# Performance work log

Measured on AMD Instinct MI355X. Metric: run time of the kernel, lower is better.

## Reference

```python
import jax, jax.numpy as jnp
import numpy as np

BS, SEQ, C = 8, 1024, 1024

def setup_inputs() -> dict:
    key = jax.random.key(0)
    ks = jax.random.split(key, 5)
    inp = {
        "input": jax.random.normal(ks[0], (BS, SEQ, C), dtype=jnp.float32),
        "Wq": jax.random.normal(ks[1], (C, C), dtype=jnp.float32) * 0.001,
        "Wk": jax.random.normal(ks[2], (C, C), dtype=jnp.float32) * 0.001,
        "Wv": jax.random.normal(ks[3], (C, C), dtype=jnp.float32) * 0.001,
        "bq": jnp.zeros((C,), dtype=jnp.float32),
        "bk": jnp.zeros((C,), dtype=jnp.float32),
        "bv": jnp.zeros((C,), dtype=jnp.float32),
        "bias_position": jnp.ones((SEQ, SEQ), dtype=jnp.float32),
    }
    return inp

def reference(input, Wq, Wk, Wv, bq, bk, bv, bias_position):
    # Linear layers (torch nn.Linear: x @ W.T + b)
    q = input @ Wq.T + bq                      # (bs, seq, c)
    k = input @ Wk.T + bk                      # (bs, seq, c)
    v = input @ Wv.T + bv                      # (bs, seq, c)
    # AFT: out[b,t,c] = sum_s exp(k[b,s,c] + bias[t,s]) * v[b,s,c]
    #                 / sum_s exp(k[b,s,c] + bias[t,s])
    # Factor exp(k + bias) = exp(bias) * exp(k) -> two GEMM-like einsums,
    # avoiding the (seq, bs, seq, c) intermediate of the original.
    ek = jnp.exp(k)                            # (bs, seq, c)
    eb = jnp.exp(bias_position)                # (t, s)
    numerator = jnp.einsum('ts,bsc->btc', eb, ek * v)   # (bs, t, c)
    denominator = jnp.einsum('ts,bsc->btc', eb, ek)     # (bs, t, c)
    out = jax.nn.sigmoid(q) * (numerator / denominator)
    return out
```

## Files before the change

kernel.cpp:

```cpp
#include <hip/hip_runtime.h>

#define BSZ 8
#define SEQL 1024
#define CHN 1024
#define M1 (BSZ*SEQL)

typedef __attribute__((ext_vector_type(8))) short bf16x8;
typedef __attribute__((ext_vector_type(4))) float f32x4;
typedef __attribute__((ext_vector_type(4))) unsigned short us4;
typedef __attribute__((ext_vector_type(8))) unsigned short us8;

static __device__ __forceinline__ unsigned short f2bf(float f){
  unsigned int u = __float_as_uint(f);
  u += 0x7fffu + ((u >> 16) & 1u);
  return (unsigned short)(u >> 16);
}
static __device__ __forceinline__ float bf2f(unsigned short h){
  return __uint_as_float(((unsigned int)h) << 16);
}
static __device__ __forceinline__ void gload16(const void* g, void* l){
  __builtin_amdgcn_global_load_lds((const __attribute__((address_space(1))) void*)g,
                                   (__attribute__((address_space(3))) void*)l,
                                   16, 0, 0);
}

__global__ void prep_kernel(const float* __restrict__ x, const float* __restrict__ wq,
                            const float* __restrict__ wk, const float* __restrict__ wv,
                            const float* __restrict__ bias,
                            unsigned short* __restrict__ xb, unsigned short* __restrict__ wqb,
                            unsigned short* __restrict__ wkb, unsigned short* __restrict__ wvb,
                            unsigned short* __restrict__ ebb)
{
  const int NX = M1 * CHN;
  const int NW = CHN * CHN;
  const int total4 = (NX + 3 * NW + SEQL * SEQL) >> 2;
  for (int i = blockIdx.x * blockDim.x + threadIdx.x; i < total4;
       i += gridDim.x * blockDim.x) {
    int e = i << 2;
    const float* src; unsigned short* dst; int off; bool ex = false;
    if (e < NX)               { src = x;    dst = xb;  off = e; }
    else if (e < NX + NW)     { src = wq;   dst = wqb; off = e - NX; }
    else if (e < NX + 2 * NW) { src = wk;   dst = wkb; off = e - (NX + NW); }
    else if (e < NX + 3 * NW) { src = wv;   dst = wvb; off = e - (NX + 2 * NW); }
    else                      { src = bias; dst = ebb; off = e - (NX + 3 * NW); ex = true; }
    float4 v = *reinterpret_cast<const float4*>(src + off);
    if (ex) { v.x = expf(v.x); v.y = expf(v.y); v.z = expf(v.z); v.w = expf(v.w); }
    us4 o; o.x = f2bf(v.x); o.y = f2bf(v.y); o.z = f2bf(v.z); o.w = f2bf(v.w);
    *reinterpret_cast<us4*>(dst + off) = o;
  }
}

__global__ __launch_bounds__(256) void gemm_qkv(
    const unsigned short* __restrict__ Xb,
    const unsigned short* __restrict__ Wq, const unsigned short* __restrict__ Wk,
    const unsigned short* __restrict__ Wv,
    const float* __restrict__ bq, const float* __restrict__ bk,
    const float* __restrict__ bv,
    unsigned short* __restrict__ Qb,
    unsigned short* __restrict__ EKT, unsigned short* __restrict__ EKVT)
{
  __shared__ unsigned short lds[20480];
  const int tid = threadIdx.x;
  const int lane = tid & 63;
  const int wm = tid >> 7;
  const int wn = (tid >> 6) & 1;
  const int nwg = gridDim.x;
  const int lid = blockIdx.x;
  const int sid = (lid & 7) * (nwg >> 3) + (lid >> 3);
  const int m0 = (sid >> 4) * 128;
  const int n0 = (sid & 15) * 64;

  const unsigned short* srcA[4]; unsigned short* dstA[4];
#pragma unroll
  for (int p = 0; p < 4; p++) {
    int l = p * 4096 + tid * 16;
    int row = l >> 7;
    int lc = ((l >> 4) & 7) ^ (row & 7);
    srcA[p] = Xb + (m0 + row) * CHN + lc * 8;
    dstA[p] = lds + (l >> 1);
  }
  const unsigned short* Ws0 = Wq; const unsigned short* Ws1 = Wk; const unsigned short* Ws2 = Wv;
  const unsigned short* srcB[3][2]; unsigned short* dstB[3][2];
#pragma unroll
  for (int w = 0; w < 3; w++) {
    const unsigned short* W = (w == 0) ? Ws0 : (w == 1) ? Ws1 : Ws2;
#pragma unroll
    for (int p = 0; p < 2; p++) {
      int l = p * 4096 + tid * 16;
      int row = l >> 7;
      int lc = ((l >> 4) & 7) ^ (row & 7);
      srcB[w][p] = W + (n0 + row) * CHN + lc * 8;
      dstB[w][p] = lds + 8192 + w * 4096 + (l >> 1);
    }
  }

  int aOff[4][2], bOff[2][2];
#pragma unroll
  for (int mi = 0; mi < 4; mi++) {
    int r = wm * 64 + mi * 16 + (lane & 15);
#pragma unroll
    for (int ks = 0; ks < 2; ks++)
      aOff[mi][ks] = r * 64 + ((((ks << 2) + (lane >> 4)) ^ (r & 7)) << 3);
  }
#pragma unroll
  for (int ni = 0; ni < 2; ni++) {
    int r = wn * 32 + ni * 16 + (lane & 15);
#pragma unroll
    for (int ks = 0; ks < 2; ks++)
      bOff[ni][ks] = r * 64 + ((((ks << 2) + (lane >> 4)) ^ (r & 7)) << 3);
  }

  f32x4 accq[4][2] = {}, acck[4][2] = {}, accv[4][2] = {};

  for (int kk = 0; kk < CHN; kk += 64) {
#pragma unroll
    for (int p = 0; p < 4; p++) gload16(srcA[p] + kk, dstA[p]);
#pragma unroll
    for (int w = 0; w < 3; w++)
#pragma unroll
      for (int p = 0; p < 2; p++) gload16(srcB[w][p] + kk, dstB[w][p]);
    __syncthreads();
#pragma unroll
    for (int ks = 0; ks < 2; ks++) {
      bf16x8 af[4];
#pragma unroll
      for (int mi = 0; mi < 4; mi++)
        af[mi] = *reinterpret_cast<const bf16x8*>(lds + aOff[mi][ks]);
#pragma unroll
      for (int ni = 0; ni < 2; ni++) {
        bf16x8 bq_ = *reinterpret_cast<const bf16x8*>(lds + 8192 + bOff[ni][ks]);
        bf16x8 bk_ = *reinterpret_cast<const bf16x8*>(lds + 12288 + bOff[ni][ks]);
        bf16x8 bv_ = *reinterpret_cast<const bf16x8*>(lds + 16384 + bOff[ni][ks]);
#pragma unroll
        for (int mi = 0; mi < 4; mi++) {
          accq[mi][ni] = __builtin_amdgcn_mfma_f32_16x16x32_bf16(af[mi], bq_, accq[mi][ni], 0, 0, 0);
          acck[mi][ni] = __builtin_amdgcn_mfma_f32_16x16x32_bf16(af[mi], bk_, acck[mi][ni], 0, 0, 0);
          accv[mi][ni] = __builtin_amdgcn_mfma_f32_16x16x32_bf16(af[mi], bv_, accv[mi][ni], 0, 0, 0);
        }
      }
    }
    __syncthreads();
  }

  const int bIdx = m0 >> 10;
  const int s0 = m0 & 1023;
  const int rb = (lane >> 4) * 4;
  float bqv[2], bkv[2], bvv[2];
#pragma unroll
  for (int ni = 0; ni < 2; ni++) {
    int c = n0 + wn * 32 + ni * 16 + (lane & 15);
    bqv[ni] = bq[c]; bkv[ni] = bk[c]; bvv[ni] = bv[c];
  }
#pragma unroll
  for (int mi = 0; mi < 4; mi++)
#pragma unroll
    for (int ni = 0; ni < 2; ni++) {
      int col = n0 + wn * 32 + ni * 16 + (lane & 15);
#pragma unroll
      for (int r = 0; r < 4; r++) {
        int mrow = m0 + wm * 64 + mi * 16 + rb + r;
        Qb[mrow * CHN + col] = f2bf(accq[mi][ni][r] + bqv[ni]);
        float ekf = expf(acck[mi][ni][r] + bkv[ni]);
        acck[mi][ni][r] = ekf;
        accv[mi][ni][r] = ekf * (accv[mi][ni][r] + bvv[ni]);
      }
    }
#pragma unroll
  for (int mi = 0; mi < 4; mi++)
#pragma unroll
    for (int ni = 0; ni < 2; ni++) {
      int nloc = wn * 32 + ni * 16 + (lane & 15);
#pragma unroll
      for (int r = 0; r < 4; r++)
        lds[nloc * 136 + wm * 64 + mi * 16 + rb + r] = f2bf(acck[mi][ni][r]);
    }
  __syncthreads();
#pragma unroll
  for (int it = 0; it < 4; it++) {
    int ch = it * 256 + tid;
    int nloc = ch >> 4, c8 = ch & 15;
    us8 v = *reinterpret_cast<const us8*>(lds + nloc * 136 + c8 * 8);
    *reinterpret_cast<us8*>(EKT + (bIdx * CHN + n0 + nloc) * SEQL + s0 + c8 * 8) = v;
  }
  __syncthreads();
#pragma unroll
  for (int mi = 0; mi < 4; mi++)
#pragma unroll
    for (int ni = 0; ni < 2; ni++) {
      int nloc = wn * 32 + ni * 16 + (lane & 15);
#pragma unroll
      for (int r = 0; r < 4; r++)
        lds[nloc * 136 + wm * 64 + mi * 16 + rb + r] = f2bf(accv[mi][ni][r]);
    }
  __syncthreads();
#pragma unroll
  for (int it = 0; it < 4; it++) {
    int ch = it * 256 + tid;
    int nloc = ch >> 4, c8 = ch & 15;
    us8 v = *reinterpret_cast<const us8*>(lds + nloc * 136 + c8 * 8);
    *reinterpret_cast<us8*>(EKVT + (bIdx * CHN + n0 + nloc) * SEQL + s0 + c8 * 8) = v;
  }
}

__global__ __launch_bounds__(256) void gemm_aft(
    const unsigned short* __restrict__ EB,
    const unsigned short* __restrict__ EKT, const unsigned short* __restrict__ EKVT,
    const unsigned short* __restrict__ Qb, float* __restrict__ out)
{
  __shared__ unsigned short lds[16384];
  const int tid = threadIdx.x;
  const int lane = tid & 63;
  const int wm = tid >> 7;
  const int wn = (tid >> 6) & 1;
  const int nwg = gridDim.x;
  const int lid = blockIdx.x;
  const int sid = (lid & 7) * (nwg >> 3) + (lid >> 3);
  const int t0 = (sid & 7) * 128;
  const int n0 = (sid >> 3) * 64;

  const unsigned short* srcA[4]; unsigned short* dstA[4];
#pragma unroll
  for (int p = 0; p < 4; p++) {
    int l = p * 4096 + tid * 16;
    int row = l >> 7;
    int lc = ((l >> 4) & 7) ^ (row & 7);
    srcA[p] = EB + (t0 + row) * SEQL + lc * 8;
    dstA[p] = lds + (l >> 1);
  }
  const unsigned short* srcB[2][2]; unsigned short* dstB[2][2];
#pragma unroll
  for (int w = 0; w < 2; w++) {
    const unsigned short* B = (w == 0) ? EKT : EKVT;
#pragma unroll
    for (int p = 0; p < 2; p++) {
      int l = p * 4096 + tid * 16;
      int row = l >> 7;
      int lc = ((l >> 4) & 7) ^ (row & 7);
      srcB[w][p] = B + (n0 + row) * SEQL + lc * 8;
      dstB[w][p] = lds + 8192 + w * 4096 + (l >> 1);
    }
  }

  int aOff[4][2], bOff[2][2];
#pragma unroll
  for (int mi = 0; mi < 4; mi++) {
    int r = wm * 64 + mi * 16 + (lane & 15);
#pragma unroll
    for (int ks = 0; ks < 2; ks++)
      aOff[mi][ks] = r * 64 + ((((ks << 2) + (lane >> 4)) ^ (r & 7)) << 3);
  }
#pragma unroll
  for (int ni = 0; ni < 2; ni++) {
    int r = wn * 32 + ni * 16 + (lane & 15);
#pragma unroll
    for (int ks = 0; ks < 2; ks++)
      bOff[ni][ks] = r * 64 + ((((ks << 2) + (lane >> 4)) ^ (r & 7)) << 3);
  }

  f32x4 accd[4][2] = {}, accn[4][2] = {};

  for (int kk = 0; kk < SEQL; kk += 64) {
#pragma unroll
    for (int p = 0; p < 4; p++) gload16(srcA[p] + kk, dstA[p]);
#pragma unroll
    for (int w = 0; w < 2; w++)
#pragma unroll
      for (int p = 0; p < 2; p++) gload16(srcB[w][p] + kk, dstB[w][p]);
    __syncthreads();
#pragma unroll
    for (int ks = 0; ks < 2; ks++) {
      bf16x8 af[4];
#pragma unroll
      for (int mi = 0; mi < 4; mi++)
        af[mi] = *reinterpret_cast<const bf16x8*>(lds + aOff[mi][ks]);
#pragma unroll
      for (int ni = 0; ni < 2; ni++) {
        bf16x8 bd_ = *reinterpret_cast<const bf16x8*>(lds + 8192 + bOff[ni][ks]);
        bf16x8 bn_ = *reinterpret_cast<const bf16x8*>(lds + 12288 + bOff[ni][ks]);
#pragma unroll
        for (int mi = 0; mi < 4; mi++) {
          accd[mi][ni] = __builtin_amdgcn_mfma_f32_16x16x32_bf16(af[mi], bd_, accd[mi][ni], 0, 0, 0);
          accn[mi][ni] = __builtin_amdgcn_mfma_f32_16x16x32_bf16(af[mi], bn_, accn[mi][ni], 0, 0, 0);
        }
      }
    }
    __syncthreads();
  }

  const int rb = (lane >> 4) * 4;
#pragma unroll
  for (int mi = 0; mi < 4; mi++)
#pragma unroll
    for (int ni = 0; ni < 2; ni++) {
      int nloc = wn * 32 + ni * 16 + (lane & 15);
      int n = n0 + nloc;
      int b = n >> 10, c = n & 1023;
#pragma unroll
      for (int r = 0; r < 4; r++) {
        int t = t0 + wm * 64 + mi * 16 + rb + r;
        float qv = bf2f(Qb[(b * SEQL + t) * CHN + c]);
        float sig = 1.0f / (1.0f + expf(-qv));
        out[(b * SEQL + t) * CHN + c] = sig * accn[mi][ni][r] / accd[mi][ni][r];
      }
    }
}

extern "C" void kernel_launch(void* const* d_in, const int* in_sizes, int n_in,
                              void* d_out, int out_size, void* d_ws, size_t ws_size,
                              hipStream_t stream) {
  (void)in_sizes; (void)n_in; (void)out_size; (void)ws_size;
  const float* x    = (const float*)d_in[0];
  const float* wq   = (const float*)d_in[1];
  const float* wk   = (const float*)d_in[2];
  const float* wv   = (const float*)d_in[3];
  const float* bq   = (const float*)d_in[4];
  const float* bk   = (const float*)d_in[5];
  const float* bv   = (const float*)d_in[6];
  const float* bias = (const float*)d_in[7];
  float* out = (float*)d_out;

  char* ws = (char*)d_ws;
  const size_t MB = 1024 * 1024;
  unsigned short* Xb   = (unsigned short*)(ws);
  unsigned short* Wqb  = (unsigned short*)(ws + 16 * MB);
  unsigned short* Wkb  = (unsigned short*)(ws + 18 * MB);
  unsigned short* Wvb  = (unsigned short*)(ws + 20 * MB);
  unsigned short* EBb  = (unsigned short*)(ws + 22 * MB);
  unsigned short* Qb   = (unsigned short*)(ws + 24 * MB);
  unsigned short* EKT  = (unsigned short*)(ws + 40 * MB);
  unsigned short* EKVT = (unsigned short*)(ws + 56 * MB);

  prep_kernel<<<2048, 256, 0, stream>>>(x, wq, wk, wv, bias, Xb, Wqb, Wkb, Wvb, EBb);
  gemm_qkv<<<1024, 256, 0, stream>>>(Xb, Wqb, Wkb, Wvb, bq, bk, bv, Qb, EKT, EKVT);
  gemm_aft<<<1024, 256, 0, stream>>>(EBb, EKT, EKVT, Qb, out);
}
```

Before: 202.7 us.

## Double-buffer LDS and use 8 waves per block in both GEMMs

Both GEMM kernels move from 4 to 8 waves per block, so each wave owns a 32x32 sub-tile instead of 64x32. The LDS staging buffers are doubled, so the next K-tile's global-to-LDS loads are issued while the current tile is being computed, with explicit vmcnt waits and raw barriers. MFMA sections are wrapped in setprio raises. The risks are more LDS per block (which may lower occupancy), and less register reuse of fragments per wave.

```diff
diff --git a/kernel.cpp b/kernel.cpp
--- a/kernel.cpp
+++ b/kernel.cpp
@@ -23,6 +23,11 @@
                                    (__attribute__((address_space(3))) void*)l,
                                    16, 0, 0);
 }
+
+#define SBAR() do { __builtin_amdgcn_sched_barrier(0); __builtin_amdgcn_s_barrier(); __builtin_amdgcn_sched_barrier(0); } while (0)
+#define LGKM0() asm volatile("s_waitcnt lgkmcnt(0)" ::: "memory")
+#define PRIO_HI() do { __builtin_amdgcn_s_setprio(1); __builtin_amdgcn_sched_barrier(0); } while (0)
+#define PRIO_LO() do { __builtin_amdgcn_sched_barrier(0); __builtin_amdgcn_s_setprio(0); } while (0)
 
 __global__ void prep_kernel(const float* __restrict__ x, const float* __restrict__ wq,
                             const float* __restrict__ wk, const float* __restrict__ wv,
@@ -50,7 +55,7 @@
   }
 }
 
-__global__ __launch_bounds__(256) void gemm_qkv(
+__global__ __launch_bounds__(512, 2) void gemm_qkv(
     const unsigned short* __restrict__ Xb,
     const unsigned short* __restrict__ Wq, const unsigned short* __restrict__ Wk,
     const unsigned short* __restrict__ Wv,
@@ -59,45 +64,44 @@
     unsigned short* __restrict__ Qb,
     unsigned short* __restrict__ EKT, unsigned short* __restrict__ EKVT)
 {
-  __shared__ unsigned short lds[20480];
+  __shared__ unsigned short lds[2 * 20480];
   const int tid = threadIdx.x;
   const int lane = tid & 63;
-  const int wm = tid >> 7;
-  const int wn = (tid >> 6) & 1;
+  const int wid = tid >> 6;
+  const int wm = wid >> 1;
+  const int wn = wid & 1;
   const int nwg = gridDim.x;
   const int lid = blockIdx.x;
   const int sid = (lid & 7) * (nwg >> 3) + (lid >> 3);
   const int m0 = (sid >> 4) * 128;
   const int n0 = (sid & 15) * 64;
 
-  const unsigned short* srcA[4]; unsigned short* dstA[4];
-#pragma unroll
-  for (int p = 0; p < 4; p++) {
-    int l = p * 4096 + tid * 16;
+  const unsigned short* srcA[2]; int dA[2];
+#pragma unroll
+  for (int p = 0; p < 2; p++) {
+    int l = p * 8192 + tid * 16;
     int row = l >> 7;
     int lc = ((l >> 4) & 7) ^ (row & 7);
     srcA[p] = Xb + (m0 + row) * CHN + lc * 8;
-    dstA[p] = lds + (l >> 1);
-  }
-  const unsigned short* Ws0 = Wq; const unsigned short* Ws1 = Wk; const unsigned short* Ws2 = Wv;
-  const unsigned short* srcB[3][2]; unsigned short* dstB[3][2];
-#pragma unroll
-  for (int w = 0; w < 3; w++) {
-    const unsigned short* W = (w == 0) ? Ws0 : (w == 1) ? Ws1 : Ws2;
-#pragma unroll
-    for (int p = 0; p < 2; p++) {
-      int l = p * 4096 + tid * 16;
-      int row = l >> 7;
-      int lc = ((l >> 4) & 7) ^ (row & 7);
-      srcB[w][p] = W + (n0 + row) * CHN + lc * 8;
-      dstB[w][p] = lds + 8192 + w * 4096 + (l >> 1);
-    }
-  }
-
-  int aOff[4][2], bOff[2][2];
-#pragma unroll
-  for (int mi = 0; mi < 4; mi++) {
-    int r = wm * 64 + mi * 16 + (lane & 15);
+    dA[p] = l >> 1;
+  }
+  const unsigned short* srcB[3]; int dB[3];
+  {
+    int l = tid * 16;
+    int row = l >> 7;
+    int lc = ((l >> 4) & 7) ^ (row & 7);
+#pragma unroll
+    for (int w = 0; w < 3; w++) {
+      const unsigned short* W = (w == 0) ? Wq : (w == 1) ? Wk : Wv;
+      srcB[w] = W + (n0 + row) * CHN + lc * 8;
+      dB[w] = 8192 + w * 4096 + (l >> 1);
+    }
+  }
+
+  int aOff[2][2], bOff[2][2];
+#pragma unroll
+  for (int mi = 0; mi < 2; mi++) {
+    int r = wm * 32 + mi * 16 + (lane & 15);
 #pragma unroll
     for (int ks = 0; ks < 2; ks++)
       aOff[mi][ks] = r * 64 + ((((ks << 2) + (lane >> 4)) ^ (r & 7)) << 3);
@@ -110,41 +114,59 @@
       bOff[ni][ks] = r * 64 + ((((ks << 2) + (lane >> 4)) ^ (r & 7)) << 3);
   }
 
-  f32x4 accq[4][2] = {}, acck[4][2] = {}, accv[4][2] = {};
-
-  for (int kk = 0; kk < CHN; kk += 64) {
-#pragma unroll
-    for (int p = 0; p < 4; p++) gload16(srcA[p] + kk, dstA[p]);
-#pragma unroll
-    for (int w = 0; w < 3; w++)
-#pragma unroll
-      for (int p = 0; p < 2; p++) gload16(srcB[w][p] + kk, dstB[w][p]);
-    __syncthreads();
+  f32x4 accq[2][2] = {}, acck[2][2] = {}, accv[2][2] = {};
+
+#pragma unroll
+  for (int p = 0; p < 2; p++) gload16(srcA[p], lds + dA[p]);
+#pragma unroll
+  for (int w = 0; w < 3; w++) gload16(srcB[w], lds + dB[w]);
+
+  for (int t = 0; t < 16; ++t) {
+    const int cur = (t & 1) * 20480;
+    const int nxt = 20480 - cur;
+    const int kn = (t + 1) << 6;
+    if (t < 15) {
+#pragma unroll
+      for (int p = 0; p < 2; p++) gload16(srcA[p] + kn, lds + nxt + dA[p]);
+      asm volatile("s_waitcnt vmcnt(2)" ::: "memory");
+    } else {
+      asm volatile("s_waitcnt vmcnt(0)" ::: "memory");
+    }
+    SBAR();
 #pragma unroll
     for (int ks = 0; ks < 2; ks++) {
-      bf16x8 af[4];
-#pragma unroll
-      for (int mi = 0; mi < 4; mi++)
-        af[mi] = *reinterpret_cast<const bf16x8*>(lds + aOff[mi][ks]);
+      bf16x8 af[2], bqf[2], bkf[2], bvf[2];
+#pragma unroll
+      for (int mi = 0; mi < 2; mi++)
+        af[mi] = *reinterpret_cast<const bf16x8*>(lds + cur + aOff[mi][ks]);
 #pragma unroll
       for (int ni = 0; ni < 2; ni++) {
-        bf16x8 bq_ = *reinterpret_cast<const bf16x8*>(lds + 8192 + bOff[ni][ks]);
-        bf16x8 bk_ = *reinterpret_cast<const bf16x8*>(lds + 12288 + bOff[ni][ks]);
-        bf16x8 bv_ = *reinterpret_cast<const bf16x8*>(lds + 16384 + bOff[ni][ks]);
-#pragma unroll
-        for (int mi = 0; mi < 4; mi++) {
-          accq[mi][ni] = __builtin_amdgcn_mfma_f32_16x16x32_bf16(af[mi], bq_, accq[mi][ni], 0, 0, 0);
-          acck[mi][ni] = __builtin_amdgcn_mfma_f32_16x16x32_bf16(af[mi], bk_, acck[mi][ni], 0, 0, 0);
-          accv[mi][ni] = __builtin_amdgcn_mfma_f32_16x16x32_bf16(af[mi], bv_, accv[mi][ni], 0, 0, 0);
+        bqf[ni] = *reinterpret_cast<const bf16x8*>(lds + cur + 8192  + bOff[ni][ks]);
+        bkf[ni] = *reinterpret_cast<const bf16x8*>(lds + cur + 12288 + bOff[ni][ks]);
+        bvf[ni] = *reinterpret_cast<const bf16x8*>(lds + cur + 16384 + bOff[ni][ks]);
+      }
+      PRIO_HI();
+#pragma unroll
+      for (int ni = 0; ni < 2; ni++)
+#pragma unroll
+        for (int mi = 0; mi < 2; mi++) {
+          accq[mi][ni] = __builtin_amdgcn_mfma_f32_16x16x32_bf16(af[mi], bqf[ni], accq[mi][ni], 0, 0, 0);
+          acck[mi][ni] = __builtin_amdgcn_mfma_f32_16x16x32_bf16(af[mi], bkf[ni], acck[mi][ni], 0, 0, 0);
+          accv[mi][ni] = __builtin_amdgcn_mfma_f32_16x16x32_bf16(af[mi], bvf[ni], accv[mi][ni], 0, 0, 0);
         }
-      }
-    }
-    __syncthreads();
+      PRIO_LO();
+      if (ks == 0 && t < 15) {
+#pragma unroll
+        for (int w = 0; w < 3; w++) gload16(srcB[w] + kn, lds + nxt + dB[w]);
+      }
+    }
+    LGKM0();
+    SBAR();
   }
 
   const int bIdx = m0 >> 10;
   const int s0 = m0 & 1023;
-  const int rb = (lane >> 4) * 4;
+  const int rbq = (lane >> 4) * 4;
   float bqv[2], bkv[2], bvv[2];
 #pragma unroll
   for (int ni = 0; ni < 2; ni++) {
@@ -152,13 +174,13 @@
     bqv[ni] = bq[c]; bkv[ni] = bk[c]; bvv[ni] = bv[c];
   }
 #pragma unroll
-  for (int mi = 0; mi < 4; mi++)
+  for (int mi = 0; mi < 2; mi++)
 #pragma unroll
     for (int ni = 0; ni < 2; ni++) {
       int col = n0 + wn * 32 + ni * 16 + (lane & 15);
 #pragma unroll
       for (int r = 0; r < 4; r++) {
-        int mrow = m0 + wm * 64 + mi * 16 + rb + r;
+        int mrow = m0 + wm * 32 + mi * 16 + rbq + r;
         Qb[mrow * CHN + col] = f2bf(accq[mi][ni][r] + bqv[ni]);
         float ekf = expf(acck[mi][ni][r] + bkv[ni]);
         acck[mi][ni][r] = ekf;
@@ -166,85 +188,85 @@
       }
     }
 #pragma unroll
-  for (int mi = 0; mi < 4; mi++)
+  for (int mi = 0; mi < 2; mi++)
 #pragma unroll
     for (int ni = 0; ni < 2; ni++) {
       int nloc = wn * 32 + ni * 16 + (lane & 15);
 #pragma unroll
       for (int r = 0; r < 4; r++)
-        lds[nloc * 136 + wm * 64 + mi * 16 + rb + r] = f2bf(acck[mi][ni][r]);
+        lds[nloc * 136 + wm * 32 + mi * 16 + rbq + r] = f2bf(acck[mi][ni][r]);
     }
   __syncthreads();
 #pragma unroll
-  for (int it = 0; it < 4; it++) {
-    int ch = it * 256 + tid;
+  for (int it = 0; it < 2; it++) {
+    int ch = it * 512 + tid;
     int nloc = ch >> 4, c8 = ch & 15;
     us8 v = *reinterpret_cast<const us8*>(lds + nloc * 136 + c8 * 8);
     *reinterpret_cast<us8*>(EKT + (bIdx * CHN + n0 + nloc) * SEQL + s0 + c8 * 8) = v;
   }
   __syncthreads();
 #pragma unroll
-  for (int mi = 0; mi < 4; mi++)
+  for (int mi = 0; mi < 2; mi++)
 #pragma unroll
     for (int ni = 0; ni < 2; ni++) {
       int nloc = wn * 32 + ni * 16 + (lane & 15);
 #pragma unroll
       for (int r = 0; r < 4; r++)
-        lds[nloc * 136 + wm * 64 + mi * 16 + rb + r] = f2bf(accv[mi][ni][r]);
+        lds[nloc * 136 + wm * 32 + mi * 16 + rbq + r] = f2bf(accv[mi][ni][r]);
     }
   __syncthreads();
 #pragma unroll
-  for (int it = 0; it < 4; it++) {
-    int ch = it * 256 + tid;
+  for (int it = 0; it < 2; it++) {
+    int ch = it * 512 + tid;
     int nloc = ch >> 4, c8 = ch & 15;
     us8 v = *reinterpret_cast<const us8*>(lds + nloc * 136 + c8 * 8);
     *reinterpret_cast<us8*>(EKVT + (bIdx * CHN + n0 + nloc) * SEQL + s0 + c8 * 8) = v;
   }
 }
 
-__global__ __launch_bounds__(256) void gemm_aft(
+__global__ __launch_bounds__(512, 4) void gemm_aft(
     const unsigned short* __restrict__ EB,
     const unsigned short* __restrict__ EKT, const unsigned short* __restrict__ EKVT,
     const unsigned short* __restrict__ Qb, float* __restrict__ out)
 {
-  __shared__ unsigned short lds[16384];
+  __shared__ unsigned short lds[2 * 16384];
   const int tid = threadIdx.x;
   const int lane = tid & 63;
-  const int wm = tid >> 7;
-  const int wn = (tid >> 6) & 1;
+  const int wid = tid >> 6;
+  const int wm = wid >> 1;
+  const int wn = wid & 1;
   const int nwg = gridDim.x;
   const int lid = blockIdx.x;
   const int sid = (lid & 7) * (nwg >> 3) + (lid >> 3);
   const int t0 = (sid & 7) * 128;
   const int n0 = (sid >> 3) * 64;
 
-  const unsigned short* srcA[4]; unsigned short* dstA[4];
-#pragma unroll
-  for (int p = 0; p < 4; p++) {
-    int l = p * 4096 + tid * 16;
+  const unsigned short* srcA[2]; int dA[2];
+#pragma unroll
+  for (int p = 0; p < 2; p++) {
+    int l = p * 8192 + tid * 16;
     int row = l >> 7;
     int lc = ((l >> 4) & 7) ^ (row & 7);
     srcA[p] = EB + (t0 + row) * SEQL + lc * 8;
-    dstA[p] = lds + (l >> 1);
-  }
-  const unsigned short* srcB[2][2]; unsigned short* dstB[2][2];
-#pragma unroll
-  for (int w = 0; w < 2; w++) {
-    const unsigned short* B = (w == 0) ? EKT : EKVT;
-#pragma unroll
-    for (int p = 0; p < 2; p++) {
-      int l = p * 4096 + tid * 16;
-      int row = l >> 7;
-      int lc = ((l >> 4) & 7) ^ (row & 7);
-      srcB[w][p] = B + (n0 + row) * SEQL + lc * 8;
-      dstB[w][p] = lds + 8192 + w * 4096 + (l >> 1);
-    }
-  }
-
-  int aOff[4][2], bOff[2][2];
-#pragma unroll
-  for (int mi = 0; mi < 4; mi++) {
-    int r = wm * 64 + mi * 16 + (lane & 15);
+    dA[p] = l >> 1;
+  }
+  const unsigned short* srcB[2]; int dB[2];
+  {
+    int l = tid * 16;
+    int row = l >> 7;
+    int lc = ((l >> 4) & 7) ^ (row & 7);
+#pragma unroll
+    for (int w = 0; w < 2; w++) {
+      const unsigned short* B = (w == 0) ? EKT : EKVT;
+      srcB[w] = B + (n0 + row) * SEQL + lc * 8;
+      dB[w] = 8192 + w * 4096 + (l >> 1);
+    }
+  }
+
+  int aOff[2][2], bOff[2][2];
+#pragma unroll
+  for (int mi = 0; mi < 2; mi++) {
+    int r = wm * 32 + mi * 16 + (lane & 15);
 #pragma unroll
     for (int ks = 0; ks < 2; ks++)
       aOff[mi][ks] = r * 64 + ((((ks << 2) + (lane >> 4)) ^ (r & 7)) << 3);
@@ -257,39 +279,57 @@
       bOff[ni][ks] = r * 64 + ((((ks << 2) + (lane >> 4)) ^ (r & 7)) << 3);
   }
 
-  f32x4 accd[4][2] = {}, accn[4][2] = {};
-
-  for (int kk = 0; kk < SEQL; kk += 64) {
-#pragma unroll
-    for (int p = 0; p < 4; p++) gload16(srcA[p] + kk, dstA[p]);
-#pragma unroll
-    for (int w = 0; w < 2; w++)
-#pragma unroll
-      for (int p = 0; p < 2; p++) gload16(srcB[w][p] + kk, dstB[w][p]);
-    __syncthreads();
+  f32x4 accd[2][2] = {}, accn[2][2] = {};
+
+#pragma unroll
+  for (int p = 0; p < 2; p++) gload16(srcA[p], lds + dA[p]);
+#pragma unroll
+  for (int w = 0; w < 2; w++) gload16(srcB[w], lds + dB[w]);
+
+  for (int t = 0; t < 16; ++t) {
+    const int cur = (t & 1) * 16384;
+    const int nxt = 16384 - cur;
+    const int kn = (t + 1) << 6;
+    if (t < 15) {
+#pragma unroll
+      for (int p = 0; p < 2; p++) gload16(srcA[p] + kn, lds + nxt + dA[p]);
+      asm volatile("s_waitcnt vmcnt(2)" ::: "memory");
+    } else {
+      asm volatile("s_waitcnt vmcnt(0)" ::: "memory");
+    }
+    SBAR();
 #pragma unroll
     for (int ks = 0; ks < 2; ks++) {
-      bf16x8 af[4];
-#pragma unroll
-      for (int mi = 0; mi < 4; mi++)
-        af[mi] = *reinterpret_cast<const bf16x8*>(lds + aOff[mi][ks]);
+      bf16x8 af[2], bdf[2], bnf[2];
+#pragma unroll
+      for (int mi = 0; mi < 2; mi++)
+        af[mi] = *reinterpret_cast<const bf16x8*>(lds + cur + aOff[mi][ks]);
 #pragma unroll
       for (int ni = 0; ni < 2; ni++) {
-        bf16x8 bd_ = *reinterpret_cast<const bf16x8*>(lds + 8192 + bOff[ni][ks]);
-        bf16x8 bn_ = *reinterpret_cast<const bf16x8*>(lds + 12288 + bOff[ni][ks]);
-#pragma unroll
-        for (int mi = 0; mi < 4; mi++) {
-          accd[mi][ni] = __builtin_amdgcn_mfma_f32_16x16x32_bf16(af[mi], bd_, accd[mi][ni], 0, 0, 0);
-          accn[mi][ni] = __builtin_amdgcn_mfma_f32_16x16x32_bf16(af[mi], bn_, accn[mi][ni], 0, 0, 0);
+        bdf[ni] = *reinterpret_cast<const bf16x8*>(lds + cur + 8192  + bOff[ni][ks]);
+        bnf[ni] = *reinterpret_cast<const bf16x8*>(lds + cur + 12288 + bOff[ni][ks]);
+      }
+      PRIO_HI();
+#pragma unroll
+      for (int ni = 0; ni < 2; ni++)
+#pragma unroll
+        for (int mi = 0; mi < 2; mi++) {
+          accd[mi][ni] = __builtin_amdgcn_mfma_f32_16x16x32_bf16(af[mi], bdf[ni], accd[mi][ni], 0, 0, 0);
+          accn[mi][ni] = __builtin_amdgcn_mfma_f32_16x16x32_bf16(af[mi], bnf[ni], accn[mi][ni], 0, 0, 0);
         }
-      }
-    }
-    __syncthreads();
-  }
-
-  const int rb = (lane >> 4) * 4;
-#pragma unroll
-  for (int mi = 0; mi < 4; mi++)
+      PRIO_LO();
+      if (ks == 0 && t < 15) {
+#pragma unroll
+        for (int w = 0; w < 2; w++) gload16(srcB[w] + kn, lds + nxt + dB[w]);
+      }
+    }
+    LGKM0();
+    SBAR();
+  }
+
+  const int rbq = (lane >> 4) * 4;
+#pragma unroll
+  for (int mi = 0; mi < 2; mi++)
 #pragma unroll
     for (int ni = 0; ni < 2; ni++) {
       int nloc = wn * 32 + ni * 16 + (lane & 15);
@@ -297,7 +337,7 @@
       int b = n >> 10, c = n & 1023;
 #pragma unroll
       for (int r = 0; r < 4; r++) {
-        int t = t0 + wm * 64 + mi * 16 + rb + r;
+        int t = t0 + wm * 32 + mi * 16 + rbq + r;
         float qv = bf2f(Qb[(b * SEQL + t) * CHN + c]);
         float sig = 1.0f / (1.0f + expf(-qv));
         out[(b * SEQL + t) * CHN + c] = sig * accn[mi][ni][r] / accd[mi][ni][r];
@@ -331,6 +371,6 @@
   unsigned short* EKVT = (unsigned short*)(ws + 56 * MB);
 
   prep_kernel<<<2048, 256, 0, stream>>>(x, wq, wk, wv, bias, Xb, Wqb, Wkb, Wvb, EBb);
-  gemm_qkv<<<1024, 256, 0, stream>>>(Xb, Wqb, Wkb, Wvb, bq, bk, bv, Qb, EKT, EKVT);
-  gemm_aft<<<1024, 256, 0, stream>>>(EBb, EKT, EKVT, Qb, out);
-}
+  gemm_qkv<<<1024, 512, 0, stream>>>(Xb, Wqb, Wkb, Wvb, bq, bk, bv, Qb, EKT, EKVT);
+  gemm_aft<<<1024, 512, 0, stream>>>(EBb, EKT, EKVT, Qb, out);
+}
```

New measurement: 194.7 us. -4.0%, faster.
